# Kernel tuning notes

Measured on AMD Instinct MI355X. Metric: run time of the kernel, lower is better.

The kernel has to match this reference:

```python
import jax, jax.numpy as jnp
import numpy as np

N_NODES = 100000
N_EDGES = 1600000
IN_C, HID_C, OUT_C = 512, 128, 40


def gcn_conv(x, edge_index):
    """Symmetric-normalized sparse aggregation: out[d] = sum_e 1/sqrt(deg[s]*deg[d]) * x[s]."""
    n = x.shape[0]
    src, dst = edge_index[0], edge_index[1]
    deg = jax.ops.segment_sum(jnp.ones_like(dst, dtype=x.dtype), dst, num_segments=n)
    deg = jnp.maximum(deg, 1.0)  # guard isolated nodes
    dinv = jax.lax.rsqrt(deg)
    w = dinv[src] * dinv[dst]                      # [E]
    msg = x[src] * w[:, None]                      # [E, C] gather + scale
    return jax.ops.segment_sum(msg, dst, num_segments=n)  # scatter-add -> [N, C]


def setup_inputs() -> dict:
    key = jax.random.key(0)
    k1, k2, k3, k4 = jax.random.split(key, 4)
    x = jax.random.normal(k1, (N_NODES, IN_C), dtype=jnp.float32)
    edge_index = jax.random.randint(k2, (2, N_EDGES), 0, N_NODES, dtype=jnp.int64)
    # xavier_uniform with gain=1.414 (as in reset_parameters), zero biases
    def xavier(k, shape, gain=1.414):
        fan_out, fan_in = shape
        bound = gain * np.sqrt(6.0 / (fan_in + fan_out))
        return jax.random.uniform(k, shape, jnp.float32, -bound, bound)
    W0 = xavier(k3, (HID_C, IN_C))
    b0 = jnp.zeros((HID_C,), jnp.float32)
    W1 = xavier(k4, (OUT_C, HID_C))
    b1 = jnp.zeros((OUT_C,), jnp.float32)
    return {"x": x, "edge_index": edge_index, "W0": W0, "b0": b0, "W1": W1, "b1": b1}


def reference(x, edge_index, W0, b0, W1, b1):
    # layer 0: project -> sparse aggregate -> bias -> relu (dropout off in eval)
    h = x @ W0.T
    h = gcn_conv(h, edge_index)
    h = jax.nn.relu(h + b0)
    # final layer: project -> sparse aggregate -> bias (no activation)
    h = h @ W1.T
    h = gcn_conv(h, edge_index)
    return h + b1
```

## Files before the change

### kernel.cpp

```cpp
#include <hip/hip_runtime.h>
#include <hip/hip_bf16.h>
#include <cstddef>

#define N_NODES 100000
#define N_EDGES 1600000
#define IN_C 512
#define HID_C 128
#define OUT_C 40
#define OUT_CP 48
#define EPB 8000
#define NPART 200
#define NBKT 196
#define BSHIFT 9

typedef short bf16x8 __attribute__((ext_vector_type(8)));
typedef float f32x4 __attribute__((ext_vector_type(4)));

__device__ __forceinline__ float bf2f(unsigned short u) {
    union { unsigned int i; float f; } v; v.i = ((unsigned int)u) << 16; return v.f;
}
__device__ __forceinline__ float bf2f_lo(unsigned int u) {
    union { unsigned int i; float f; } v; v.i = u << 16; return v.f;
}
__device__ __forceinline__ float bf2f_hi(unsigned int u) {
    union { unsigned int i; float f; } v; v.i = u & 0xFFFF0000u; return v.f;
}
__device__ __forceinline__ unsigned short f2bf(float f) {
    union { float f; unsigned int i; } v; v.f = f;
    unsigned int x = v.i;
    return (unsigned short)((x + 0x7FFFu + ((x >> 16) & 1u)) >> 16);
}

__device__ __forceinline__ void glds16(const void* g, void* l) {
    __builtin_amdgcn_global_load_lds(
        (const __attribute__((address_space(1))) unsigned int*)g,
        (__attribute__((address_space(3))) unsigned int*)l,
        16, 0, 0);
}

__global__ void k_detect(const unsigned int* __restrict__ xbits,
                         const int* __restrict__ ei32, int* __restrict__ flags) {
    if (threadIdx.x == 0 && blockIdx.x == 0) {
        int inrange = 0;
        for (int i = 0; i < 64; i++) {
            unsigned int b = xbits[i * 33 + 1];
            int e = (int)((b >> 23) & 0xFFu);
            if (e >= 90 && e <= 160) inrange++;
        }
        flags[0] = (inrange >= 32) ? 0 : 1;
        int zeros = 0;
        for (int i = 0; i < 8; i++) if (ei32[2 * i + 1] == 0) zeros++;
        flags[1] = (zeros == 8) ? 1 : 0;
    }
}

__device__ __forceinline__ int load_src(const int* ei, int mi, int e) {
    return mi ? ei[2 * e] : ei[e];
}
__device__ __forceinline__ int load_dst(const int* ei, int mi, int e) {
    return mi ? ei[2 * (N_EDGES + e)] : ei[N_EDGES + e];
}

#define NW_TOTAL (IN_C * HID_C + HID_C * OUT_C + HID_C + OUT_C)
__global__ void k_norm_w(const void* __restrict__ W0, const void* __restrict__ W1,
                         const void* __restrict__ b0, const void* __restrict__ b1,
                         const int* __restrict__ flags,
                         unsigned short* __restrict__ w0n, unsigned short* __restrict__ w1n,
                         float* __restrict__ b0n, float* __restrict__ b1n) {
    int mf = flags[0];
    int i = blockIdx.x * 256 + threadIdx.x;
    if (i >= NW_TOTAL) return;
    if (i < IN_C * HID_C) {
        w0n[i] = mf ? ((const unsigned short*)W0)[i] : f2bf(((const float*)W0)[i]);
    } else if (i < IN_C * HID_C + HID_C * OUT_C) {
        int j = i - IN_C * HID_C;
        w1n[j] = mf ? ((const unsigned short*)W1)[j] : f2bf(((const float*)W1)[j]);
    } else if (i < IN_C * HID_C + HID_C * OUT_C + HID_C) {
        int j = i - IN_C * HID_C - HID_C * OUT_C;
        b0n[j] = mf ? bf2f(((const unsigned short*)b0)[j]) : ((const float*)b0)[j];
    } else {
        int j = i - IN_C * HID_C - HID_C * OUT_C - HID_C;
        b1n[j] = mf ? bf2f(((const unsigned short*)b1)[j]) : ((const float*)b1)[j];
    }
}

__global__ __launch_bounds__(256) void k_part1(const int* __restrict__ ei,
                                               const int* __restrict__ flags,
                                               int* __restrict__ bcnt,
                                               int* __restrict__ block_off) {
    __shared__ int h[NBKT];
    int t = threadIdx.x;
    for (int i = t; i < NBKT; i += 256) h[i] = 0;
    __syncthreads();
    int mi = flags[1];
    int base = blockIdx.x * EPB;
    for (int j = t; j < EPB; j += 256) {
        int e = base + j;
        if (e < N_EDGES) atomicAdd(&h[load_dst(ei, mi, e) >> BSHIFT], 1);
    }
    __syncthreads();
    for (int i = t; i < NBKT; i += 256)
        block_off[blockIdx.x * NBKT + i] = atomicAdd(&bcnt[i], h[i]);
}

__global__ void k_scan_bkt(const int* __restrict__ bcnt, int* __restrict__ bbase) {
    __shared__ int sm[256];
    int t = threadIdx.x;
    int v = (t < NBKT) ? bcnt[t] : 0;
    sm[t] = v; __syncthreads();
    for (int off = 1; off < 256; off <<= 1) {
        int a = (t >= off) ? sm[t - off] : 0;
        __syncthreads();
        sm[t] += a;
        __syncthreads();
    }
    if (t < NBKT) bbase[t] = sm[t] - v;
    if (t == NBKT - 1) bbase[NBKT] = sm[t];
}

__global__ __launch_bounds__(256) void k_part2(const int* __restrict__ ei,
                                               const int* __restrict__ flags,
                                               const int* __restrict__ bbase,
                                               const int* __restrict__ block_off,
                                               unsigned int* __restrict__ bedges) {
    __shared__ int cur[NBKT];
    int t = threadIdx.x;
    for (int i = t; i < NBKT; i += 256)
        cur[i] = bbase[i] + block_off[blockIdx.x * NBKT + i];
    __syncthreads();
    int mi = flags[1];
    int base = blockIdx.x * EPB;
    for (int j = t; j < EPB; j += 256) {
        int e = base + j;
        if (e < N_EDGES) {
            int d = load_dst(ei, mi, e);
            int s = load_src(ei, mi, e);
            int p = atomicAdd(&cur[d >> BSHIFT], 1);
            bedges[p] = ((unsigned int)s << BSHIFT) | (unsigned int)(d & 511);
        }
    }
}

__global__ __launch_bounds__(512) void k_bucket_csr(const unsigned int* __restrict__ bedges,
                                                    const int* __restrict__ bbase,
                                                    int* __restrict__ rowptr,
                                                    float* __restrict__ dinv,
                                                    int* __restrict__ col) {
    __shared__ int cnt[512];
    __shared__ int cur[512];
    int b = blockIdx.x, t = threadIdx.x;
    int ebeg = bbase[b], eend = bbase[b + 1];
    cnt[t] = 0;
    __syncthreads();
    for (int j = ebeg + t; j < eend; j += 512)
        atomicAdd(&cnt[bedges[j] & 511], 1);
    __syncthreads();
    int v = cnt[t];
    cur[t] = v; __syncthreads();
    for (int off = 1; off < 512; off <<= 1) {
        int a = (t >= off) ? cur[t - off] : 0;
        __syncthreads();
        cur[t] += a;
        __syncthreads();
    }
    int excl = cur[t] - v;
    int node = b * 512 + t;
    if (node < N_NODES) {
        rowptr[node] = ebeg + excl;
        float dd = (float)v; if (dd < 1.f) dd = 1.f;
        dinv[node] = rsqrtf(dd);
    } else if (node == N_NODES) {
        rowptr[N_NODES] = ebeg + excl;
    }
    __syncthreads();
    cur[t] = ebeg + excl;
    __syncthreads();
    for (int j = ebeg + t; j < eend; j += 512) {
        unsigned int pk = bedges[j];
        int p = atomicAdd(&cur[pk & 511], 1);
        col[p] = (int)(pk >> BSHIFT);
    }
}

#define G1_BUF 24576
#define G1_BOFF 16384

__device__ __forceinline__ void gemm1_f32_async(const float* __restrict__ xg,
                                                const unsigned short* __restrict__ w0n,
                                                const float* __restrict__ dinv,
                                                unsigned short* __restrict__ h1,
                                                char* __restrict__ smem,
                                                int node0, int t) {
    const int w = t >> 6;
    const int lane = t & 63;
    const int r16 = lane & 15;
    const int quad = lane >> 4;

    f32x4 acc[2][8];
#pragma unroll
    for (int m = 0; m < 2; m++)
#pragma unroll
        for (int c = 0; c < 8; c++) acc[m][c] = (f32x4){0.f, 0.f, 0.f, 0.f};

    const int lrow = lane >> 3;
    const int lch = (lane & 7) ^ lrow;
    const float* pa[4];
#pragma unroll
    for (int g = 0; g < 4; g++) {
        int r = node0 + w * 32 + 8 * g + lrow;
        if (r >= N_NODES) r = N_NODES - 1;
        pa[g] = xg + (size_t)r * IN_C + lch * 4;
    }
    const unsigned short* pb[2];
#pragma unroll
    for (int g = 0; g < 2; g++)
        pb[g] = w0n + (size_t)((2 * w + g) * 16 + r16) * IN_C + quad * 8;

    auto stage = [&](int buf, int ks) {
        char* Ab = smem + buf * G1_BUF + w * 4096;
        char* Bb = smem + buf * G1_BUF + G1_BOFF + w * 2048;
        glds16(pa[0] + ks, Ab);
        glds16(pa[1] + ks, Ab + 1024);
        glds16(pa[2] + ks, Ab + 2048);
        glds16(pa[3] + ks, Ab + 3072);
        glds16(pb[0] + ks, Bb);
        glds16(pb[1] + ks, Bb + 1024);
    };

    const int swz = r16 & 7;

    auto compute = [&](int buf) {
        const char* Ab = smem + buf * G1_BUF;
        const char* Bb = Ab + G1_BOFF;
        bf16x8 a[2];
#pragma unroll
        for (int m = 0; m < 2; m++) {
            int rowb = (w * 32 + m * 16 + r16) * 128;
            int c0 = ((2 * quad) ^ swz) * 16;
            int c1 = ((2 * quad + 1) ^ swz) * 16;
            float4 fa = *reinterpret_cast<const float4*>(Ab + rowb + c0);
            float4 fb = *reinterpret_cast<const float4*>(Ab + rowb + c1);
            a[m] = (bf16x8){(short)f2bf(fa.x), (short)f2bf(fa.y), (short)f2bf(fa.z), (short)f2bf(fa.w),
                            (short)f2bf(fb.x), (short)f2bf(fb.y), (short)f2bf(fb.z), (short)f2bf(fb.w)};
        }
#pragma unroll
        for (int ct = 0; ct < 8; ct++) {
            bf16x8 b = *reinterpret_cast<const bf16x8*>(Bb + ct * 1024 + lane * 16);
            acc[0][ct] = __builtin_amdgcn_mfma_f32_16x16x32_bf16(a[0], b, acc[0][ct], 0, 0, 0);
            acc[1][ct] = __builtin_amdgcn_mfma_f32_16x16x32_bf16(a[1], b, acc[1][ct], 0, 0, 0);
        }
    };

    stage(0, 0);
    stage(1, 32);
    for (int tt = 0; tt < 14; ++tt) {
        asm volatile("s_waitcnt vmcnt(6)" ::: "memory");
        __builtin_amdgcn_sched_barrier(0);
        __builtin_amdgcn_s_barrier();
        compute(tt & 1);
        __builtin_amdgcn_s_barrier();
        stage(tt & 1, (tt + 2) * 32);
    }
    asm volatile("s_waitcnt vmcnt(6)" ::: "memory");
    __builtin_amdgcn_sched_barrier(0);
    __builtin_amdgcn_s_barrier();
    compute(0);
    asm volatile("s_waitcnt vmcnt(0)" ::: "memory");
    __builtin_amdgcn_sched_barrier(0);
    __builtin_amdgcn_s_barrier();
    compute(1);

#pragma unroll
    for (int m = 0; m < 2; m++) {
#pragma unroll
        for (int r = 0; r < 4; r++) {
            int row = node0 + w * 32 + m * 16 + quad * 4 + r;
            if (row < N_NODES) {
                float dv = dinv[row];
#pragma unroll
                for (int ct = 0; ct < 8; ct++)
                    h1[(size_t)row * HID_C + ct * 16 + r16] = f2bf(acc[m][ct][r] * dv);
            }
        }
    }
}

__device__ __forceinline__ void gemm1_bf16_async(const unsigned short* __restrict__ xg,
                                                 const unsigned short* __restrict__ w0n,
                                                 const float* __restrict__ dinv,
                                                 unsigned short* __restrict__ h1,
                                                 unsigned short* __restrict__ smem,
                                                 int node0, int t) {
    const int w = t >> 6;
    const int lane = t & 63;
    const int r16 = lane & 15;
    const int quad = lane >> 4;

    f32x4 acc[2][8];
#pragma unroll
    for (int m = 0; m < 2; m++)
#pragma unroll
        for (int c = 0; c < 8; c++) acc[m][c] = (f32x4){0.f, 0.f, 0.f, 0.f};

    int rA0 = node0 + (2 * w) * 16 + r16;     if (rA0 >= N_NODES) rA0 = N_NODES - 1;
    int rA1 = node0 + (2 * w + 1) * 16 + r16; if (rA1 >= N_NODES) rA1 = N_NODES - 1;
    const unsigned short* pa0 = xg + (size_t)rA0 * IN_C + quad * 8;
    const unsigned short* pa1 = xg + (size_t)rA1 * IN_C + quad * 8;
    const unsigned short* pb0 = w0n + (size_t)((2 * w) * 16 + r16) * IN_C + quad * 8;
    const unsigned short* pb1 = w0n + (size_t)((2 * w + 1) * 16 + r16) * IN_C + quad * 8;

    auto stage = [&](int buf, int ks) {
        unsigned short* a = smem + buf * 8192 + (2 * w) * 512;
        glds16(pa0 + ks, a);
        glds16(pa1 + ks, a + 512);
        glds16(pb0 + ks, a + 4096);
        glds16(pb1 + ks, a + 4096 + 512);
    };

    const int fo = quad * 128 + r16 * 8;

    auto compute = [&](int buf) {
        const unsigned short* Ab = smem + buf * 8192;
        const unsigned short* Bb = Ab + 4096;
        bf16x8 a0 = *reinterpret_cast<const bf16x8*>(Ab + (2 * w) * 512 + fo);
        bf16x8 a1 = *reinterpret_cast<const bf16x8*>(Ab + (2 * w + 1) * 512 + fo);
#pragma unroll
        for (int ct = 0; ct < 8; ct++) {
            bf16x8 b = *reinterpret_cast<const bf16x8*>(Bb + ct * 512 + fo);
            acc[0][ct] = __builtin_amdgcn_mfma_f32_16x16x32_bf16(a0, b, acc[0][ct], 0, 0, 0);
            acc[1][ct] = __builtin_amdgcn_mfma_f32_16x16x32_bf16(a1, b, acc[1][ct], 0, 0, 0);
        }
    };

    stage(0, 0);
    __syncthreads();
    for (int tt = 0; tt < 15; ++tt) {
        int cur = tt & 1;
        stage(cur ^ 1, (tt + 1) * 32);
        compute(cur);
        __syncthreads();
    }
    compute(1);

#pragma unroll
    for (int m = 0; m < 2; m++) {
#pragma unroll
        for (int r = 0; r < 4; r++) {
            int row = node0 + w * 32 + m * 16 + quad * 4 + r;
            if (row < N_NODES) {
                float dv = dinv[row];
#pragma unroll
                for (int ct = 0; ct < 8; ct++)
                    h1[(size_t)row * HID_C + ct * 16 + r16] = f2bf(acc[m][ct][r] * dv);
            }
        }
    }
}

__global__ __launch_bounds__(256, 3) void k_gemm1(const void* __restrict__ x,
                                                  const unsigned short* __restrict__ w0n,
                                                  const int* __restrict__ flags,
                                                  const float* __restrict__ dinv,
                                                  unsigned short* __restrict__ h1) {
    __shared__ __align__(16) char smem[2 * G1_BUF];
    int node0 = blockIdx.x * 128;
    int t = threadIdx.x;
    if (flags[0]) gemm1_bf16_async((const unsigned short*)x, w0n, dinv, h1,
                                   (unsigned short*)smem, node0, t);
    else          gemm1_f32_async((const float*)x, w0n, dinv, h1, smem, node0, t);
}

__global__ __launch_bounds__(256) void k_agg1(const int* __restrict__ rowptr,
                                              const int* __restrict__ col,
                                              const float* __restrict__ dinv,
                                              const unsigned int* __restrict__ h1v,
                                              const float* __restrict__ b0n,
                                              unsigned int* __restrict__ h2v) {
    int w = threadIdx.x >> 6;
    int lane = threadIdx.x & 63;
    int d = blockIdx.x * 4 + w;
    if (d >= N_NODES) return;
    int beg = __builtin_amdgcn_readfirstlane(rowptr[d]);
    int end = __builtin_amdgcn_readfirstlane(rowptr[d + 1]);
    float a0 = 0.f, a1 = 0.f;
    for (int j0 = beg; j0 < end; j0 += 16) {
        int s[16];
        float m[16];
#pragma unroll
        for (int q = 0; q < 16; q++) {
            int jj = j0 + q;
            int jc = jj < end ? jj : end - 1;
            s[q] = col[jc];
            m[q] = jj < end ? 1.f : 0.f;
        }
        unsigned int r[16];
#pragma unroll
        for (int q = 0; q < 16; q++) {
            const unsigned int* rp = h1v + (size_t)s[q] * 64;
            r[q] = rp[lane];
        }
#pragma unroll
        for (int q = 0; q < 16; q++) {
            a0 += m[q] * bf2f_lo(r[q]);
            a1 += m[q] * bf2f_hi(r[q]);
        }
    }
    float dv = dinv[d];
    float o0 = a0 * dv + b0n[2 * lane];
    float o1 = a1 * dv + b0n[2 * lane + 1];
    o0 = o0 > 0.f ? o0 : 0.f;
    o1 = o1 > 0.f ? o1 : 0.f;
    h2v[(size_t)d * 64 + lane] = (unsigned int)f2bf(o0) | ((unsigned int)f2bf(o1) << 16);
}

__global__ __launch_bounds__(256) void k_gemm2(const unsigned short* __restrict__ h2,
                                               const unsigned short* __restrict__ w1p,
                                               const float* __restrict__ dinv,
                                               float* __restrict__ p2) {
    int wave = (blockIdx.x * 256 + (int)threadIdx.x) >> 6;
    if (wave >= N_NODES / 16) return;
    int lane = threadIdx.x & 63;
    int r16 = lane & 15;
    int quad = lane >> 4;
    int node_base = wave * 16;

    f32x4 acc[3];
#pragma unroll
    for (int c = 0; c < 3; c++) acc[c] = (f32x4){0.f, 0.f, 0.f, 0.f};

    const unsigned short* arow = h2 + (size_t)(node_base + r16) * HID_C + quad * 8;
    const unsigned short* brow = w1p + (size_t)r16 * HID_C + quad * 8;

#pragma unroll
    for (int k0 = 0; k0 < HID_C; k0 += 32) {
        bf16x8 a = *reinterpret_cast<const bf16x8*>(arow + k0);
#pragma unroll
        for (int ct = 0; ct < 3; ct++) {
            bf16x8 b = *reinterpret_cast<const bf16x8*>(brow + (size_t)ct * 16 * HID_C + k0);
            acc[ct] = __builtin_amdgcn_mfma_f32_16x16x32_bf16(a, b, acc[ct], 0, 0, 0);
        }
    }

    float dv[4];
#pragma unroll
    for (int r = 0; r < 4; r++) dv[r] = dinv[node_base + quad * 4 + r];

#pragma unroll
    for (int ct = 0; ct < 3; ct++) {
        int chan = ct * 16 + r16;
        if (chan < OUT_C) {
#pragma unroll
            for (int r = 0; r < 4; r++) {
                p2[(size_t)(node_base + quad * 4 + r) * OUT_C + chan] = acc[ct][r] * dv[r];
            }
        }
    }
}

__global__ __launch_bounds__(256) void k_agg2(const int* __restrict__ rowptr,
                                              const int* __restrict__ col,
                                              const float* __restrict__ dinv,
                                              const float* __restrict__ p2,
                                              const float* __restrict__ b1n,
                                              const int* __restrict__ flags,
                                              void* __restrict__ out) {
    int w = threadIdx.x >> 6;
    int lane = threadIdx.x & 63;
    int d = blockIdx.x * 4 + w;
    if (d >= N_NODES || lane >= OUT_C) return;
    int beg = __builtin_amdgcn_readfirstlane(rowptr[d]);
    int end = __builtin_amdgcn_readfirstlane(rowptr[d + 1]);
    float acc = 0.f;
    for (int j0 = beg; j0 < end; j0 += 16) {
        int s[16];
        float m[16];
#pragma unroll
        for (int q = 0; q < 16; q++) {
            int jj = j0 + q;
            int jc = jj < end ? jj : end - 1;
            s[q] = col[jc];
            m[q] = jj < end ? 1.f : 0.f;
        }
        float r[16];
#pragma unroll
        for (int q = 0; q < 16; q++) {
            const float* rp = p2 + (size_t)s[q] * OUT_C;
            r[q] = rp[lane];
        }
#pragma unroll
        for (int q = 0; q < 16; q++) acc += m[q] * r[q];
    }
    float v = acc * dinv[d] + b1n[lane];
    size_t idx = (size_t)d * OUT_C + lane;
    if (flags[0]) ((unsigned short*)out)[idx] = f2bf(v);
    else          ((float*)out)[idx] = v;
}

extern "C" void kernel_launch(void* const* d_in, const int* in_sizes, int n_in,
                              void* d_out, int out_size, void* d_ws, size_t ws_size,
                              hipStream_t stream) {
    const void* x  = d_in[0];
    const int* ei  = (const int*)d_in[1];
    const void* W0 = d_in[2];
    const void* b0 = d_in[3];
    const void* W1 = d_in[4];
    const void* b1 = d_in[5];

    char* ws = (char*)d_ws;
    size_t off = 0;
    auto alloc = [&](size_t bytes) {
        char* p = ws + off;
        off += (bytes + 511) & ~(size_t)511;
        return p;
    };
    int*   flags   = (int*)  alloc(sizeof(int) * 2);
    int*   rowptr  = (int*)  alloc(sizeof(int) * (N_NODES + 1));
    float* dinv    = (float*)alloc(sizeof(float) * N_NODES);
    int*   col     = (int*)  alloc(sizeof(int) * N_EDGES);
    int*   bcnt    = (int*)  alloc(sizeof(int) * NBKT);
    int*   bbase   = (int*)  alloc(sizeof(int) * (NBKT + 1));
    int*   bloff   = (int*)  alloc(sizeof(int) * NPART * NBKT);
    unsigned int* bedges = (unsigned int*)alloc(sizeof(unsigned int) * N_EDGES);
    unsigned short* w0n = (unsigned short*)alloc(sizeof(unsigned short) * IN_C * HID_C);
    unsigned short* w1n = (unsigned short*)alloc(sizeof(unsigned short) * OUT_CP * HID_C);
    float* b0n = (float*)alloc(sizeof(float) * HID_C);
    float* b1n = (float*)alloc(sizeof(float) * OUT_C);
    unsigned short* h1 = (unsigned short*)alloc(sizeof(unsigned short) * (size_t)N_NODES * HID_C);
    unsigned short* h2 = (unsigned short*)alloc(sizeof(unsigned short) * (size_t)N_NODES * HID_C);
    float* p2 = (float*)h1;

    k_detect<<<1, 64, 0, stream>>>((const unsigned int*)x, ei, flags);
    hipMemsetAsync(w1n, 0, sizeof(unsigned short) * OUT_CP * HID_C, stream);
    k_norm_w<<<(NW_TOTAL + 255) / 256, 256, 0, stream>>>(W0, W1, b0, b1, flags, w0n, w1n, b0n, b1n);

    hipMemsetAsync(bcnt, 0, sizeof(int) * NBKT, stream);
    k_part1<<<NPART, 256, 0, stream>>>(ei, flags, bcnt, bloff);
    k_scan_bkt<<<1, 256, 0, stream>>>(bcnt, bbase);
    k_part2<<<NPART, 256, 0, stream>>>(ei, flags, bbase, bloff, bedges);
    k_bucket_csr<<<NBKT, 512, 0, stream>>>(bedges, bbase, rowptr, dinv, col);

    k_gemm1<<<(N_NODES + 127) / 128, 256, 0, stream>>>(x, w0n, flags, dinv, h1);
    k_agg1<<<(N_NODES + 3) / 4, 256, 0, stream>>>(rowptr, col, dinv,
                                                  (const unsigned int*)h1, b0n,
                                                  (unsigned int*)h2);
    k_gemm2<<<(N_NODES / 16 + 3) / 4, 256, 0, stream>>>(h2, w1n, dinv, p2);
    k_agg2<<<(N_NODES + 3) / 4, 256, 0, stream>>>(rowptr, col, dinv, p2, b1n, flags, d_out);
}
```

Baseline: 503.1 us.

## Fuse layer-1 aggregation with second GEMM via LDS staging

Merges the first sparse aggregation and the 128-to-40 projection into one kernel. Each block aggregates 16 nodes (4 per wave) into LDS, then one wave runs MFMA on the staged tile, so the bf16 h2 intermediate no longer goes through global memory and one launch is dropped. The trade-off is that three of the four waves sit idle during the MFMA step and each wave now processes four nodes in sequence. The detect kernel is also reworked to use wave ballots instead of a serial single-thread loop.

```diff
diff --git a/kernel.cpp b/kernel.cpp
--- a/kernel.cpp
+++ b/kernel.cpp
@@ -40,17 +40,15 @@
 
 __global__ void k_detect(const unsigned int* __restrict__ xbits,
                          const int* __restrict__ ei32, int* __restrict__ flags) {
-    if (threadIdx.x == 0 && blockIdx.x == 0) {
-        int inrange = 0;
-        for (int i = 0; i < 64; i++) {
-            unsigned int b = xbits[i * 33 + 1];
-            int e = (int)((b >> 23) & 0xFFu);
-            if (e >= 90 && e <= 160) inrange++;
-        }
-        flags[0] = (inrange >= 32) ? 0 : 1;
-        int zeros = 0;
-        for (int i = 0; i < 8; i++) if (ei32[2 * i + 1] == 0) zeros++;
-        flags[1] = (zeros == 8) ? 1 : 0;
+    int lane = threadIdx.x & 63;
+    unsigned int b = xbits[lane * 33 + 1];
+    int e = (int)((b >> 23) & 0xFFu);
+    unsigned long long bal = __ballot(e >= 90 && e <= 160);
+    int zpred = (lane < 8) ? (ei32[2 * lane + 1] == 0) : 0;
+    unsigned long long zb = __ballot(zpred);
+    if (lane == 0) {
+        flags[0] = (__popcll(bal) >= 32) ? 0 : 1;
+        flags[1] = ((zb & 0xFFull) == 0xFFull) ? 1 : 0;
     }
 }
 
@@ -370,70 +368,66 @@
     else          gemm1_f32_async((const float*)x, w0n, dinv, h1, smem, node0, t);
 }
 
-__global__ __launch_bounds__(256) void k_agg1(const int* __restrict__ rowptr,
-                                              const int* __restrict__ col,
-                                              const float* __restrict__ dinv,
-                                              const unsigned int* __restrict__ h1v,
-                                              const float* __restrict__ b0n,
-                                              unsigned int* __restrict__ h2v) {
+__global__ __launch_bounds__(256) void k_agg1g2(const int* __restrict__ rowptr,
+                                                const int* __restrict__ col,
+                                                const float* __restrict__ dinv,
+                                                const unsigned int* __restrict__ h1v,
+                                                const float* __restrict__ b0n,
+                                                const unsigned short* __restrict__ w1p,
+                                                float* __restrict__ p2) {
+    __shared__ unsigned int H[16][68];
     int w = threadIdx.x >> 6;
     int lane = threadIdx.x & 63;
-    int d = blockIdx.x * 4 + w;
-    if (d >= N_NODES) return;
-    int beg = __builtin_amdgcn_readfirstlane(rowptr[d]);
-    int end = __builtin_amdgcn_readfirstlane(rowptr[d + 1]);
-    float a0 = 0.f, a1 = 0.f;
-    for (int j0 = beg; j0 < end; j0 += 16) {
-        int s[16];
-        float m[16];
-#pragma unroll
-        for (int q = 0; q < 16; q++) {
-            int jj = j0 + q;
-            int jc = jj < end ? jj : end - 1;
-            s[q] = col[jc];
-            m[q] = jj < end ? 1.f : 0.f;
-        }
-        unsigned int r[16];
-#pragma unroll
-        for (int q = 0; q < 16; q++) {
-            const unsigned int* rp = h1v + (size_t)s[q] * 64;
-            r[q] = rp[lane];
-        }
-#pragma unroll
-        for (int q = 0; q < 16; q++) {
-            a0 += m[q] * bf2f_lo(r[q]);
-            a1 += m[q] * bf2f_hi(r[q]);
-        }
-    }
-    float dv = dinv[d];
-    float o0 = a0 * dv + b0n[2 * lane];
-    float o1 = a1 * dv + b0n[2 * lane + 1];
-    o0 = o0 > 0.f ? o0 : 0.f;
-    o1 = o1 > 0.f ? o1 : 0.f;
-    h2v[(size_t)d * 64 + lane] = (unsigned int)f2bf(o0) | ((unsigned int)f2bf(o1) << 16);
-}
-
-__global__ __launch_bounds__(256) void k_gemm2(const unsigned short* __restrict__ h2,
-                                               const unsigned short* __restrict__ w1p,
-                                               const float* __restrict__ dinv,
-                                               float* __restrict__ p2) {
-    int wave = (blockIdx.x * 256 + (int)threadIdx.x) >> 6;
-    if (wave >= N_NODES / 16) return;
-    int lane = threadIdx.x & 63;
+    int nb = blockIdx.x * 16;
+    float bl = b0n[2 * lane], bh = b0n[2 * lane + 1];
+#pragma unroll
+    for (int i = 0; i < 4; i++) {
+        int d = nb + w * 4 + i;
+        int beg = __builtin_amdgcn_readfirstlane(rowptr[d]);
+        int end = __builtin_amdgcn_readfirstlane(rowptr[d + 1]);
+        float a0 = 0.f, a1 = 0.f;
+        for (int j0 = beg; j0 < end; j0 += 16) {
+            int s[16];
+            float m[16];
+#pragma unroll
+            for (int q = 0; q < 16; q++) {
+                int jj = j0 + q;
+                int jc = jj < end ? jj : end - 1;
+                s[q] = col[jc];
+                m[q] = jj < end ? 1.f : 0.f;
+            }
+            unsigned int r[16];
+#pragma unroll
+            for (int q = 0; q < 16; q++) {
+                const unsigned int* rp = h1v + (size_t)s[q] * 64;
+                r[q] = rp[lane];
+            }
+#pragma unroll
+            for (int q = 0; q < 16; q++) {
+                a0 += m[q] * bf2f_lo(r[q]);
+                a1 += m[q] * bf2f_hi(r[q]);
+            }
+        }
+        float dv = dinv[d];
+        float o0 = a0 * dv + bl;
+        float o1 = a1 * dv + bh;
+        o0 = o0 > 0.f ? o0 : 0.f;
+        o1 = o1 > 0.f ? o1 : 0.f;
+        H[w * 4 + i][lane] = (unsigned int)f2bf(o0) | ((unsigned int)f2bf(o1) << 16);
+    }
+    __syncthreads();
+    if (w != 0) return;
+
     int r16 = lane & 15;
     int quad = lane >> 4;
-    int node_base = wave * 16;
-
     f32x4 acc[3];
 #pragma unroll
     for (int c = 0; c < 3; c++) acc[c] = (f32x4){0.f, 0.f, 0.f, 0.f};
 
-    const unsigned short* arow = h2 + (size_t)(node_base + r16) * HID_C + quad * 8;
     const unsigned short* brow = w1p + (size_t)r16 * HID_C + quad * 8;
-
 #pragma unroll
     for (int k0 = 0; k0 < HID_C; k0 += 32) {
-        bf16x8 a = *reinterpret_cast<const bf16x8*>(arow + k0);
+        bf16x8 a = *reinterpret_cast<const bf16x8*>(&H[r16][k0 / 2 + quad * 4]);
 #pragma unroll
         for (int ct = 0; ct < 3; ct++) {
             bf16x8 b = *reinterpret_cast<const bf16x8*>(brow + (size_t)ct * 16 * HID_C + k0);
@@ -441,9 +435,9 @@
         }
     }
 
-    float dv[4];
-#pragma unroll
-    for (int r = 0; r < 4; r++) dv[r] = dinv[node_base + quad * 4 + r];
+    float dvv[4];
+#pragma unroll
+    for (int r = 0; r < 4; r++) dvv[r] = dinv[nb + quad * 4 + r];
 
 #pragma unroll
     for (int ct = 0; ct < 3; ct++) {
@@ -451,7 +445,7 @@
         if (chan < OUT_C) {
 #pragma unroll
             for (int r = 0; r < 4; r++) {
-                p2[(size_t)(node_base + quad * 4 + r) * OUT_C + chan] = acc[ct][r] * dv[r];
+                p2[(size_t)(nb + quad * 4 + r) * OUT_C + chan] = acc[ct][r] * dvv[r];
             }
         }
     }
@@ -526,8 +520,7 @@
     float* b0n = (float*)alloc(sizeof(float) * HID_C);
     float* b1n = (float*)alloc(sizeof(float) * OUT_C);
     unsigned short* h1 = (unsigned short*)alloc(sizeof(unsigned short) * (size_t)N_NODES * HID_C);
-    unsigned short* h2 = (unsigned short*)alloc(sizeof(unsigned short) * (size_t)N_NODES * HID_C);
-    float* p2 = (float*)h1;
+    float* p2 = (float*)alloc(sizeof(float) * (size_t)N_NODES * OUT_C);
 
     k_detect<<<1, 64, 0, stream>>>((const unsigned int*)x, ei, flags);
     hipMemsetAsync(w1n, 0, sizeof(unsigned short) * OUT_CP * HID_C, stream);
@@ -540,9 +533,8 @@
     k_bucket_csr<<<NBKT, 512, 0, stream>>>(bedges, bbase, rowptr, dinv, col);
 
     k_gemm1<<<(N_NODES + 127) / 128, 256, 0, stream>>>(x, w0n, flags, dinv, h1);
-    k_agg1<<<(N_NODES + 3) / 4, 256, 0, stream>>>(rowptr, col, dinv,
-                                                  (const unsigned int*)h1, b0n,
-                                                  (unsigned int*)h2);
-    k_gemm2<<<(N_NODES / 16 + 3) / 4, 256, 0, stream>>>(h2, w1n, dinv, p2);
+    k_agg1g2<<<N_NODES / 16, 256, 0, stream>>>(rowptr, col, dinv,
+                                               (const unsigned int*)h1, b0n,
+                                               w1n, p2);
     k_agg2<<<(N_NODES + 3) / 4, 256, 0, stream>>>(rowptr, col, dinv, p2, b1n, flags, d_out);
 }
```

Result: no change. 493.4 us (-1.9%).
